# Kernel optimization log

Measured on AMD Instinct MI355X. Metric: run time of the kernel, lower is better.

## Reference

```python
import jax, jax.numpy as jnp
import numpy as np

B, S, V, E, HE, HD, MEL_D, MEL_T = 4096, 13, 276, 128, 256, 256, 80, 250

def setup_inputs() -> dict:
    key = jax.random.key(0)
    ks = jax.random.split(key, 20)
    p = lambda k, sh: (jax.random.normal(k, sh, dtype=jnp.float32) * 0.05)
    return {
        'text': jax.random.randint(ks[0], (B, S), 0, V),
        'surprisal': jax.random.normal(ks[1], (B, S), dtype=jnp.float32),
        'emb': p(ks[2], (V, E)),
        'sw': p(ks[3], (E, 1)), 'sb': p(ks[4], (E,)),
        'ew_ih': p(ks[5], (4 * HE, E)), 'ew_hh': p(ks[6], (4 * HE, HE)),
        'eb_ih': p(ks[7], (4 * HE,)), 'eb_hh': p(ks[8], (4 * HE,)),
        'aw': p(ks[9], (1, HD + HE)), 'ab': p(ks[10], (1,)),
        'dw_ih': p(ks[11], (4 * HD, E + HE)), 'dw_hh': p(ks[12], (4 * HD, HD)),
        'db_ih': p(ks[13], (4 * HD,)), 'db_hh': p(ks[14], (4 * HD,)),
        'f1w': p(ks[15], (1024, S * HD)), 'f1b': p(ks[16], (1024,)),
        'f2w': p(ks[17], (MEL_D * MEL_T, 1024)), 'f2b': p(ks[18], (MEL_D * MEL_T,)),
        'init_in': jnp.zeros((E,), dtype=jnp.float32),
    }

def _lstm_cell(x, h, c, w_ih, w_hh, b_ih, b_hh, H):
    # PyTorch gate order: i, f, g, o
    g = x @ w_ih.T + b_ih + h @ w_hh.T + b_hh
    i, f, gg, o = jnp.split(g, 4, axis=-1)
    c2 = jax.nn.sigmoid(f) * c + jax.nn.sigmoid(i) * jnp.tanh(gg)
    h2 = jax.nn.sigmoid(o) * jnp.tanh(c2)
    return h2, c2

def reference(text, surprisal, emb, sw, sb, ew_ih, ew_hh, eb_ih, eb_hh,
              aw, ab, dw_ih, dw_hh, db_ih, db_hh, f1w, f1b, f2w, f2b, init_in):
    # embedding + surprisal projection
    x = emb[text] + (surprisal[..., None] @ sw.T + sb)  # [B,S,E]

    # encoder LSTM over time
    def enc_step(carry, xt):
        h, c = carry
        h2, c2 = _lstm_cell(xt, h, c, ew_ih, ew_hh, eb_ih, eb_hh, HE)
        return (h2, c2), h2
    h0 = jnp.zeros((B, HE), dtype=x.dtype)
    (h_n, c_n), enc_seq = jax.lax.scan(enc_step, (h0, h0), jnp.swapaxes(x, 0, 1))
    enc_out = jnp.swapaxes(enc_seq, 0, 1)  # [B,S,HE]

    # precompute encoder part of attention scores (constant across steps)
    aw_h, aw_e = aw[0, :HD], aw[0, HD:]
    enc_score = enc_out @ aw_e + ab[0]  # [B,S]

    dec_in = jnp.broadcast_to(init_in, (B, E))

    def dec_step(carry, _):
        h, c = carry
        scores = h @ aw_h + 0.0  # [B]
        w = jax.nn.softmax(scores[:, None] + enc_score, axis=1)  # [B,S]
        context = jnp.einsum('bs,bsh->bh', w, enc_out)
        xcat = jnp.concatenate([dec_in, context], axis=-1)
        h2, c2 = _lstm_cell(xcat, h, c, dw_ih, dw_hh, db_ih, db_hh, HD)
        return (h2, c2), h2
    _, dec_seq = jax.lax.scan(dec_step, (h_n, c_n), None, length=S)
    dec_out = jnp.swapaxes(dec_seq, 0, 1).reshape(B, S * HD)  # [B,13*256]

    hfc = jax.nn.relu(dec_out @ f1w.T + f1b)
    out = (hfc @ f2w.T + f2b).reshape(B, MEL_D, MEL_T)
    return out
```

## Files before the change

kernel.cpp:

```cpp
#include <hip/hip_runtime.h>
#include <hip/hip_bf16.h>
#include <stdint.h>
#include <stddef.h>

#define B 4096
#define S 13
#define NG 1024
#define MEL 20000
#define MELP 20480

typedef __attribute__((ext_vector_type(8))) short bf16x8;
typedef __attribute__((ext_vector_type(4))) float f32x4;

__device__ __forceinline__ void g2l16(void* lds, const void* g) {
    __builtin_amdgcn_global_load_lds(
        (const __attribute__((address_space(1))) void*)g,
        (__attribute__((address_space(3))) void*)lds, 16, 0, 0);
}

__device__ __forceinline__ float sigm(float x) { return 1.0f / (1.0f + expf(-x)); }
__device__ __forceinline__ float b2f(unsigned short u) {
    union { float f; unsigned int i; } x; x.i = ((unsigned)u) << 16; return x.f;
}
__device__ __forceinline__ unsigned short f2bu(float f) {
    __hip_bfloat16 h = __float2bfloat16(f);
    return *reinterpret_cast<unsigned short*>(&h);
}
__device__ __forceinline__ bf16x8 cvt8(f32x4 a, f32x4 b) {
    union { bf16x8 v; __hip_bfloat16 e[8]; } u;
    #pragma unroll
    for (int j = 0; j < 4; ++j) { u.e[j] = __float2bfloat16(a[j]); u.e[4 + j] = __float2bfloat16(b[j]); }
    return u.v;
}

__device__ __forceinline__ void swz_decode(int wg, int nwg, int nx, int& bx, int& by) {
    const int cpx = nwg >> 3;
    wg = (wg & 7) * cpx + (wg >> 3);
    const int gsz = nx * 4;
    const int grp = wg / gsz, rem = wg % gsz;
    by = grp * 4 + (rem & 3);
    bx = rem >> 2;
}

#define BAR() do { asm volatile("" ::: "memory"); \
    __builtin_amdgcn_s_barrier(); \
    __builtin_amdgcn_sched_barrier(0); } while (0)

#define P_DECL() \
    __shared__ __hip_bfloat16 As3[4][128 * 32]; \
    __shared__ __hip_bfloat16 Bs3[4][64 * 32]; \
    const int tid  = threadIdx.x; \
    const int lane = tid & 63; \
    const int wv   = tid >> 6; \
    const int l16  = lane & 15; \
    const int sr   = tid >> 2; \
    const int sc   = (((tid & 3) ^ ((tid >> 3) & 3)) << 3); \
    const int sl   = (((lane >> 4) ^ ((l16 >> 1) & 3)) << 3)

#define STG3(buf, k0) do { \
    g2l16(&As3[buf][sr * 32 + (tid & 3) * 8],         Ag + (size_t)sr * K + (k0) + sc); \
    g2l16(&As3[buf][(sr + 64) * 32 + (tid & 3) * 8],  Ag + (size_t)(sr + 64) * K + (k0) + sc); \
    g2l16(&Bs3[buf][sr * 32 + (tid & 3) * 8],         Wg + (size_t)sr * K + (k0) + sc); } while (0)

#define TILE3(cur, stg, k2, DO_STG) do { \
    const __hip_bfloat16* Ab = As3[cur]; \
    const __hip_bfloat16* Bb = Bs3[cur]; \
    bf16x8 af[2], bfr[4]; \
    _Pragma("unroll") for (int m = 0; m < 2; ++m) \
        af[m] = *(const bf16x8*)(Ab + (wv * 32 + m * 16 + l16) * 32 + sl); \
    _Pragma("unroll") for (int n = 0; n < 4; ++n) \
        bfr[n] = *(const bf16x8*)(Bb + (n * 16 + l16) * 32 + sl); \
    if (DO_STG) STG3(stg, k2); \
    __builtin_amdgcn_s_setprio(1); \
    _Pragma("unroll") for (int m = 0; m < 2; ++m) \
        _Pragma("unroll") for (int n = 0; n < 4; ++n) \
            acc[m][n] = __builtin_amdgcn_mfma_f32_16x16x32_bf16(af[m], bfr[n], acc[m][n], 0, 0, 0); \
    __builtin_amdgcn_s_setprio(0); \
} while (0)

#define PIPELINE(K) do { \
    const int nk = (K) >> 5; \
    STG3(0, 0); \
    STG3(1, 32); \
    STG3(2, 64); \
    asm volatile("s_waitcnt vmcnt(6)" ::: "memory"); \
    BAR(); \
    int cur = 0; \
    for (int t = 0; t < nk - 3; ++t) { \
        const int stg = (cur + 3) & 3; \
        TILE3(cur, stg, (t + 3) << 5, true); \
        asm volatile("s_waitcnt vmcnt(6)" ::: "memory"); \
        BAR(); \
        cur = (cur + 1) & 3; \
    } \
    TILE3(cur, 0, 0, false); \
    asm volatile("s_waitcnt vmcnt(3)" ::: "memory"); \
    BAR(); \
    cur = (cur + 1) & 3; \
    TILE3(cur, 0, 0, false); \
    asm volatile("s_waitcnt vmcnt(0)" ::: "memory"); \
    BAR(); \
    cur = (cur + 1) & 3; \
    TILE3(cur, 0, 0, false); \
} while (0)

__global__ __launch_bounds__(256, 2) void gemm3(
    const __hip_bfloat16* __restrict__ A,
    const __hip_bfloat16* __restrict__ W,
    const float* __restrict__ bias,
    float* __restrict__ Cf,
    __hip_bfloat16* __restrict__ Cbf,
    int N, int K, int ldc, int relu, int nx)
{
    P_DECL();
    int bx, by;
    swz_decode(blockIdx.x, gridDim.x, nx, bx, by);
    const int brow = by * 128, bcol = bx * 64;
    const __hip_bfloat16* Ag = A + (size_t)brow * K;
    const __hip_bfloat16* Wg = W + (size_t)bcol * K;
    f32x4 acc[2][4] = {};

    PIPELINE(K);

    const int r4 = (lane >> 4) * 4;
    #pragma unroll
    for (int m = 0; m < 2; ++m) {
        #pragma unroll
        for (int n = 0; n < 4; ++n) {
            const int col = bcol + n * 16 + l16;
            if (col >= N) continue;
            const float bv = bias ? bias[col] : 0.0f;
            #pragma unroll
            for (int r = 0; r < 4; ++r) {
                const int row = brow + wv * 32 + m * 16 + r4 + r;
                float v = acc[m][n][r] + bv;
                if (relu) v = v > 0.0f ? v : 0.0f;
                if (Cf)  Cf[(size_t)row * ldc + col] = v;
                if (Cbf) Cbf[(size_t)row * ldc + col] = __float2bfloat16(v);
            }
        }
    }
}

__global__ __launch_bounds__(256, 2) void gemm_lstm3(
    const __hip_bfloat16* __restrict__ A,
    const __hip_bfloat16* __restrict__ W,
    const float* __restrict__ bias,
    float* __restrict__ c,
    __hip_bfloat16* __restrict__ hb1, int s1,
    __hip_bfloat16* __restrict__ hb2, int s2,
    int K,
    const float* __restrict__ aw,
    float* __restrict__ score)
{
    P_DECL();
    int bx, by;
    swz_decode(blockIdx.x, gridDim.x, 16, bx, by);
    const int brow = by * 128, bcol = bx * 64;
    const __hip_bfloat16* Ag = A + (size_t)brow * K;
    const __hip_bfloat16* Wg = W + (size_t)bcol * K;
    f32x4 acc[2][4] = {};

    PIPELINE(K);

    const int r4 = (lane >> 4) * 4;
    const int unit = bx * 16 + l16;
    const float b0 = bias[bcol + l16];
    const float b1 = bias[bcol + 16 + l16];
    const float b2 = bias[bcol + 32 + l16];
    const float b3 = bias[bcol + 48 + l16];
    const float awe = score ? aw[256 + unit] : 0.0f;
    float ps[2][4];
    #pragma unroll
    for (int m = 0; m < 2; ++m) {
        #pragma unroll
        for (int r = 0; r < 4; ++r) {
            const int row = brow + wv * 32 + m * 16 + r4 + r;
            const float gi = acc[m][0][r] + b0;
            const float gf = acc[m][1][r] + b1;
            const float gg = acc[m][2][r] + b2;
            const float go = acc[m][3][r] + b3;
            const size_t ci = (size_t)row * 256 + unit;
            const float c2 = sigm(gf) * c[ci] + sigm(gi) * tanhf(gg);
            const float h2 = sigm(go) * tanhf(c2);
            c[ci] = c2;
            ps[m][r] = h2 * awe;
            const __hip_bfloat16 hb = __float2bfloat16(h2);
            hb1[(size_t)row * s1 + unit] = hb;
            hb2[(size_t)row * s2 + unit] = hb;
        }
    }
    if (score) {
        #pragma unroll
        for (int m = 0; m < 2; ++m) {
            #pragma unroll
            for (int r = 0; r < 4; ++r) {
                float v = ps[m][r];
                v += __shfl_xor(v, 1);
                v += __shfl_xor(v, 2);
                v += __shfl_xor(v, 4);
                v += __shfl_xor(v, 8);
                if (l16 == 0) {
                    const int row = brow + wv * 32 + m * 16 + r4 + r;
                    atomicAdd(&score[(size_t)row * S], v);
                }
            }
        }
    }
}

__global__ __launch_bounds__(256, 2) void gemm_lstm_dec(
    const __hip_bfloat16* __restrict__ A,
    const __hip_bfloat16* __restrict__ W,
    const float* __restrict__ gctx,
    float* __restrict__ c,
    __hip_bfloat16* __restrict__ hb1,
    __hip_bfloat16* __restrict__ hb2, int s2,
    int K)
{
    P_DECL();
    int bx, by;
    swz_decode(blockIdx.x, gridDim.x, 16, bx, by);
    const int brow = by * 128, bcol = bx * 64;
    const __hip_bfloat16* Ag = A + (size_t)brow * K;
    const __hip_bfloat16* Wg = W + (size_t)bcol * K;
    f32x4 acc[2][4] = {};

    PIPELINE(K);

    const int r4 = (lane >> 4) * 4;
    const int unit = bx * 16 + l16;
    #pragma unroll
    for (int m = 0; m < 2; ++m) {
        #pragma unroll
        for (int r = 0; r < 4; ++r) {
            const int row = brow + wv * 32 + m * 16 + r4 + r;
            const float* g = gctx + (size_t)row * NG + bcol;
            const float gi = acc[m][0][r] + g[l16];
            const float gf = acc[m][1][r] + g[16 + l16];
            const float gg = acc[m][2][r] + g[32 + l16];
            const float go = acc[m][3][r] + g[48 + l16];
            const size_t ci = (size_t)row * 256 + unit;
            const float c2 = sigm(gf) * c[ci] + sigm(gi) * tanhf(gg);
            const float h2 = sigm(go) * tanhf(c2);
            c[ci] = c2;
            const __hip_bfloat16 hb = __float2bfloat16(h2);
            hb1[(size_t)row * 256 + unit] = hb;
            hb2[(size_t)row * s2 + unit] = hb;
        }
    }
}

__global__ __launch_bounds__(512, 2) void gemm256(
    const __hip_bfloat16* __restrict__ A,
    const __hip_bfloat16* __restrict__ W,
    const float* __restrict__ bias,
    float* __restrict__ Cf,
    int N, int K, int ldc, int nx)
{
    __shared__ __hip_bfloat16 As[4][256 * 32];
    __shared__ __hip_bfloat16 Bs[4][256 * 32];
    const int tid  = threadIdx.x;
    const int lane = tid & 63;
    const int wv = tid >> 6, wr = wv >> 2, wc = wv & 3;
    const int l16 = lane & 15;
    int bx, by;
    {
        const int xcd = blockIdx.x & 7;
        const int lid = blockIdx.x >> 3;
        const int st  = lid >> 4;
        const int w   = lid & 15;
        const int gst = xcd * 10 + st;
        const int sbx = gst >> 2;
        const int sby = gst & 3;
        bx = sbx * 4 + (w & 3);
        by = sby * 4 + (w >> 2);
    }
    const int brow = by * 256, bcol = bx * 256;
    const __hip_bfloat16* Ag = A + (size_t)brow * K;
    const __hip_bfloat16* Wg = W + (size_t)bcol * K;
    const int sr = tid >> 2;
    const int sc = (((tid & 3) ^ ((tid >> 3) & 3)) << 3);
    const int sd = tid * 8;
    const int sl = (((lane >> 4) ^ ((l16 >> 1) & 3)) << 3);
    f32x4 acc[8][4] = {};
    const int nk = K >> 5;

    #define STG_A(buf, k0) do { \
        g2l16(&As[buf][sd],        Ag + (size_t)sr * K + (k0) + sc);         \
        g2l16(&As[buf][4096 + sd], Ag + (size_t)(sr + 128) * K + (k0) + sc); } while (0)
    #define STG_B(buf, k0) do { \
        g2l16(&Bs[buf][sd],        Wg + (size_t)sr * K + (k0) + sc);         \
        g2l16(&Bs[buf][4096 + sd], Wg + (size_t)(sr + 128) * K + (k0) + sc); } while (0)

    #define TILE(cur, stg, k2, DO_STG) do {                                    \
        const __hip_bfloat16* Ab = As[cur];                                    \
        const __hip_bfloat16* Bb = Bs[cur];                                    \
        bf16x8 bfr[4], af[4];                                                  \
        _Pragma("unroll") for (int n = 0; n < 4; ++n)                          \
            bfr[n] = *(const bf16x8*)(Bb + (wc * 64 + n * 16 + l16) * 32 + sl);\
        _Pragma("unroll") for (int m = 0; m < 4; ++m)                          \
            af[m] = *(const bf16x8*)(Ab + (wr * 128 + m * 16 + l16) * 32 + sl);\
        if (DO_STG) STG_A(stg, k2);                                            \
        __builtin_amdgcn_s_setprio(1);                                         \
        _Pragma("unroll") for (int m = 0; m < 4; ++m)                          \
            _Pragma("unroll") for (int n = 0; n < 4; ++n)                      \
                acc[m][n] = __builtin_amdgcn_mfma_f32_16x16x32_bf16(           \
                    af[m], bfr[n], acc[m][n], 0, 0, 0);                        \
        __builtin_amdgcn_s_setprio(0);                                         \
        _Pragma("unroll") for (int m = 0; m < 4; ++m)                          \
            af[m] = *(const bf16x8*)(Ab + (wr * 128 + (m + 4) * 16 + l16) * 32 + sl); \
        if (DO_STG) STG_B(stg, k2);                                            \
        __builtin_amdgcn_s_setprio(1);                                         \
        _Pragma("unroll") for (int m = 0; m < 4; ++m)                          \
            _Pragma("unroll") for (int n = 0; n < 4; ++n)                      \
                acc[m + 4][n] = __builtin_amdgcn_mfma_f32_16x16x32_bf16(       \
                    af[m], bfr[n], acc[m + 4][n], 0, 0, 0);                    \
        __builtin_amdgcn_s_setprio(0);                                         \
    } while (0)

    STG_A(0, 0);  STG_B(0, 0);
    STG_A(1, 32); STG_B(1, 32);
    STG_A(2, 64); STG_B(2, 64);
    asm volatile("s_waitcnt vmcnt(8)" ::: "memory");
    BAR();
    int cur = 0;
    for (int t = 0; t < nk - 3; ++t) {
        const int stg = (cur + 3) & 3;
        TILE(cur, stg, (t + 3) << 5, true);
        asm volatile("s_waitcnt vmcnt(8)" ::: "memory");
        BAR();
        cur = (cur + 1) & 3;
    }
    TILE(cur, 0, 0, false);
    asm volatile("s_waitcnt vmcnt(4)" ::: "memory");
    BAR();
    cur = (cur + 1) & 3;
    TILE(cur, 0, 0, false);
    asm volatile("s_waitcnt vmcnt(0)" ::: "memory");
    BAR();
    cur = (cur + 1) & 3;
    TILE(cur, 0, 0, false);

    const int r4 = (lane >> 4) * 4;
    #pragma unroll
    for (int m = 0; m < 8; ++m) {
        #pragma unroll
        for (int n = 0; n < 4; ++n) {
            const int col = bcol + wc * 64 + n * 16 + l16;
            if (col >= N) continue;
            const float bv = bias[col];
            #pragma unroll
            for (int r = 0; r < 4; ++r) {
                const int row = brow + wr * 128 + m * 16 + r4 + r;
                Cf[(size_t)row * ldc + col] = acc[m][n][r] + bv;
            }
        }
    }
}

__device__ __forceinline__ int unperm(int np) {
    const int u = ((np >> 6) << 4) + (np & 15);
    const int g = (np >> 4) & 3;
    return g * 256 + u;
}

#define N_W2   ((long long)MELP * 1024 / 8)
#define N_W1   ((long long)NG * 3328 / 8)
#define N_WE   ((long long)NG * 384 / 8)
#define N_WD   ((long long)NG * 512 / 8)
#define N_EMB  ((long long)B * S * 32)
#define N_INIT ((long long)B * 256)
#define N_F2B  ((long long)MELP)
#define N_BP   ((long long)NG)
#define N_ES   ((long long)B * S)
#define N_PREP (N_W2 + N_W1 + N_WE + N_WD + N_EMB + N_INIT + N_F2B + N_BP + N_ES)

__global__ void prep_all(
    const int* __restrict__ text, const float* __restrict__ surp,
    const float* __restrict__ emb, const float* __restrict__ sw,
    const float* __restrict__ sb,
    const float* __restrict__ ew_ih, const float* __restrict__ ew_hh,
    const float* __restrict__ eb_ih, const float* __restrict__ eb_hh,
    const float* __restrict__ dw_ih, const float* __restrict__ dw_hh,
    const float* __restrict__ db_ih, const float* __restrict__ db_hh,
    const float* __restrict__ f1w, const float* __restrict__ f2w,
    const float* __restrict__ f2b, const float* __restrict__ init_in,
    const float* __restrict__ ab,
    __hip_bfloat16* __restrict__ Wenc,
    __hip_bfloat16* __restrict__ Wdc, __hip_bfloat16* __restrict__ Wdh,
    __hip_bfloat16* __restrict__ W1, __hip_bfloat16* __restrict__ W2,
    float* __restrict__ f2bp, float* __restrict__ be, float* __restrict__ bd,
    __hip_bfloat16* __restrict__ xall, float* __restrict__ c_buf,
    float* __restrict__ enc_score)
{
    long long id = (long long)blockIdx.x * 256 + threadIdx.x;
    if (id < N_W2) {
        const long long i8 = id * 8;
        bf16x8 v;
        if (i8 < (long long)MEL * 1024) {
            v = cvt8(*(const f32x4*)(f2w + i8), *(const f32x4*)(f2w + i8 + 4));
        } else {
            union { bf16x8 w; __hip_bfloat16 e[8]; } u;
            #pragma unroll
            for (int j = 0; j < 8; ++j) u.e[j] = __float2bfloat16(0.0f);
            v = u.w;
        }
        *(bf16x8*)(W2 + i8) = v;
        return;
    }
    id -= N_W2;
    if (id < N_W1) {
        const long long i8 = id * 8;
        *(bf16x8*)(W1 + i8) = cvt8(*(const f32x4*)(f1w + i8), *(const f32x4*)(f1w + i8 + 4));
        return;
    }
    id -= N_W1;
    if (id < N_WE) {
        const int idx = (int)(id * 8);
        const int np = idx / 384, k = idx % 384;
        const int n = unperm(np);
        const float* src = (k < 128) ? (ew_ih + n * 128 + k) : (ew_hh + n * 256 + (k - 128));
        *(bf16x8*)(Wenc + idx) = cvt8(*(const f32x4*)src, *(const f32x4*)(src + 4));
        return;
    }
    id -= N_WE;
    if (id < N_WD) {
        const int idx = (int)(id * 8);
        const int np = idx / 512, k = idx % 512;
        const int n = unperm(np);
        if (k < 256) {
            const float* src = dw_ih + n * 384 + 128 + k;
            *(bf16x8*)(Wdc + np * 256 + k) = cvt8(*(const f32x4*)src, *(const f32x4*)(src + 4));
        } else {
            const float* src = dw_hh + n * 256 + (k - 256);
            *(bf16x8*)(Wdh + np * 256 + (k - 256)) = cvt8(*(const f32x4*)src, *(const f32x4*)(src + 4));
        }
        return;
    }
    id -= N_WD;
    if (id < N_EMB) {
        const int idx = (int)id;
        const int jj = (idx & 31) * 4;
        const int rest = idx >> 5;
        const int b = rest % B;
        const int s = rest / B;
        const float sp = surp[b * S + s];
        const f32x4 e4 = *(const f32x4*)(emb + (size_t)text[b * S + s] * 128 + jj);
        const f32x4 w4 = *(const f32x4*)(sw + jj);
        const f32x4 b4 = *(const f32x4*)(sb + jj);
        __hip_bfloat16* dst = xall + ((size_t)s * B + b) * 384 + jj;
        #pragma unroll
        for (int i = 0; i < 4; ++i) dst[i] = __float2bfloat16(e4[i] + sp * w4[i] + b4[i]);
        return;
    }
    id -= N_EMB;
    if (id < N_INIT) {
        const int idx = (int)id;
        c_buf[idx] = 0.0f;
        const int b = idx >> 8, jj = idx & 255;
        xall[(size_t)b * 384 + 128 + jj] = __float2bfloat16(0.0f);
        return;
    }
    id -= N_INIT;
    if (id < N_F2B) {
        const int idx = (int)id;
        f2bp[idx] = (idx < MEL) ? f2b[idx] : 0.0f;
        return;
    }
    id -= N_F2B;
    if (id < N_BP) {
        const int np = (int)id;
        const int n = unperm(np);
        be[np] = eb_ih[n] + eb_hh[n];
        float s = db_ih[n] + db_hh[n];
        for (int k = 0; k < 128; ++k) s += dw_ih[n * 384 + k] * init_in[k];
        bd[np] = s;
        return;
    }
    id -= N_BP;
    if (id < N_ES) {
        enc_score[id] = ab[0];
        return;
    }
}

__global__ void attn_once(const __hip_bfloat16* __restrict__ enc_out,
                          const float* __restrict__ enc_score,
                          __hip_bfloat16* __restrict__ ctx) {
    int b = (blockIdx.x * 256 + threadIdx.x) >> 6;
    int lane = threadIdx.x & 63;
    if (b >= B) return;
    float sc[S], mx = -1e30f;
    #pragma unroll
    for (int t = 0; t < S; ++t) { sc[t] = enc_score[b * S + t]; mx = fmaxf(mx, sc[t]); }
    float sum = 0.0f;
    #pragma unroll
    for (int t = 0; t < S; ++t) { sc[t] = expf(sc[t] - mx); sum += sc[t]; }
    const float inv = 1.0f / sum;
    float c0 = 0.f, c1 = 0.f, c2 = 0.f, c3 = 0.f;
    #pragma unroll
    for (int t = 0; t < S; ++t) {
        const ushort4 e4 = *(const ushort4*)(enc_out + ((size_t)b * S + t) * 256 + lane * 4);
        const float w = sc[t] * inv;
        c0 += w * b2f(e4.x); c1 += w * b2f(e4.y);
        c2 += w * b2f(e4.z); c3 += w * b2f(e4.w);
    }
    ushort4 o4 = { f2bu(c0), f2bu(c1), f2bu(c2), f2bu(c3) };
    *(ushort4*)(ctx + (size_t)b * 256 + lane * 4) = o4;
}

#define CDIV(a, b) (((a) + (b) - 1) / (b))

extern "C" void kernel_launch(void* const* d_in, const int* in_sizes, int n_in,
                              void* d_out, int out_size, void* d_ws, size_t ws_size,
                              hipStream_t stream) {
    const int*   text    = (const int*)  d_in[0];
    const float* surp    = (const float*)d_in[1];
    const float* emb     = (const float*)d_in[2];
    const float* sw      = (const float*)d_in[3];
    const float* sb      = (const float*)d_in[4];
    const float* ew_ih   = (const float*)d_in[5];
    const float* ew_hh   = (const float*)d_in[6];
    const float* eb_ih   = (const float*)d_in[7];
    const float* eb_hh   = (const float*)d_in[8];
    const float* aw      = (const float*)d_in[9];
    const float* ab      = (const float*)d_in[10];
    const float* dw_ih   = (const float*)d_in[11];
    const float* dw_hh   = (const float*)d_in[12];
    const float* db_ih   = (const float*)d_in[13];
    const float* db_hh   = (const float*)d_in[14];
    const float* f1w     = (const float*)d_in[15];
    const float* f1b     = (const float*)d_in[16];
    const float* f2w     = (const float*)d_in[17];
    const float* f2b     = (const float*)d_in[18];
    const float* init_in = (const float*)d_in[19];
    float* out = (float*)d_out;

    char* p = (char*)d_ws;
    auto alloc = [&](size_t bytes) {
        void* r = (void*)p;
        p += (bytes + 255) & ~(size_t)255;
        return r;
    };
    __hip_bfloat16* Wenc      = (__hip_bfloat16*)alloc((size_t)NG * 384 * 2);
    __hip_bfloat16* Wdc       = (__hip_bfloat16*)alloc((size_t)NG * 256 * 2);
    __hip_bfloat16* Wdh       = (__hip_bfloat16*)alloc((size_t)NG * 256 * 2);
    __hip_bfloat16* W1        = (__hip_bfloat16*)alloc((size_t)NG * 3328 * 2);
    __hip_bfloat16* W2        = (__hip_bfloat16*)alloc((size_t)MELP * 1024 * 2);
    float*          f2bp      = (float*)alloc((size_t)MELP * 4);
    float*          be        = (float*)alloc((size_t)NG * 4);
    float*          bd        = (float*)alloc((size_t)NG * 4);
    __hip_bfloat16* xall      = (__hip_bfloat16*)alloc((size_t)S * B * 384 * 2);
    __hip_bfloat16* enc_out   = (__hip_bfloat16*)alloc((size_t)B * S * 256 * 2);
    float*          enc_score = (float*)alloc((size_t)B * S * 4);
    float*          c_buf     = (float*)alloc((size_t)B * 256 * 4);
    __hip_bfloat16* ctx       = (__hip_bfloat16*)alloc((size_t)B * 256 * 2);
    float*          gctx      = (float*)alloc((size_t)B * NG * 4);
    __hip_bfloat16* hdec      = (__hip_bfloat16*)alloc((size_t)2 * B * 256 * 2);
    __hip_bfloat16* dec_out   = (__hip_bfloat16*)alloc((size_t)B * 3328 * 2);
    __hip_bfloat16* hfc       = (__hip_bfloat16*)alloc((size_t)B * 1024 * 2);
    (void)ws_size; (void)in_sizes; (void)n_in; (void)out_size;

    prep_all<<<(int)CDIV(N_PREP, 256), 256, 0, stream>>>(
        text, surp, emb, sw, sb, ew_ih, ew_hh, eb_ih, eb_hh,
        dw_ih, dw_hh, db_ih, db_hh, f1w, f2w, f2b, init_in, ab,
        Wenc, Wdc, Wdh, W1, W2, f2bp, be, bd, xall, c_buf, enc_score);

    for (int t = 0; t < S; ++t) {
        __hip_bfloat16* hb1; int s1;
        if (t < S - 1) { hb1 = xall + ((size_t)(t + 1) * B * 384) + 128; s1 = 384; }
        else           { hb1 = hdec; s1 = 256; }
        gemm_lstm3<<<512, 256, 0, stream>>>(
            xall + (size_t)t * B * 384, Wenc, be, c_buf,
            hb1, s1, enc_out + (size_t)t * 256, S * 256, 384,
            aw, enc_score + t);
    }

    attn_once<<<CDIV(B * 64, 256), 256, 0, stream>>>(enc_out, enc_score, ctx);
    gemm3<<<(NG / 64) * (B / 128), 256, 0, stream>>>(
        ctx, Wdc, bd, gctx, (__hip_bfloat16*)nullptr, NG, 256, NG, 0, NG / 64);

    for (int t = 0; t < S; ++t) {
        gemm_lstm_dec<<<512, 256, 0, stream>>>(
            hdec + (size_t)(t & 1) * B * 256, Wdh, gctx, c_buf,
            hdec + (size_t)((t + 1) & 1) * B * 256,
            dec_out + (size_t)t * 256, 3328, 256);
    }

    gemm3<<<(NG / 64) * (B / 128), 256, 0, stream>>>(
        dec_out, W1, f1b, (float*)nullptr, hfc, NG, 3328, NG, 1, NG / 64);

    gemm256<<<(MELP / 256) * (B / 256), 512, 0, stream>>>(
        hfc, W2, f2bp, out, MEL, 1024, MEL, MELP / 256);
}
```

Measured before the change: 596.9 us.

## Restructure GEMM K-loop to process tile pairs with one barrier per pair

Both GEMM main loops now prefetch four K-stages up front, then walk the K dimension two tiles at a time. Each pair restages two buffers, and a single full vmcnt(0) wait plus barrier follows the pair. The aim is to halve the number of barriers and drop the peeled epilogue tiles. The cost is that the prefetch is fully drained every two tiles, so only about one tile of compute hides each load, versus roughly three before. The loop also assumes an even number of K-tiles.

```diff
diff --git a/kernel.cpp b/kernel.cpp
--- a/kernel.cpp
+++ b/kernel.cpp
@@ -83,25 +83,18 @@
     STG3(0, 0); \
     STG3(1, 32); \
     STG3(2, 64); \
+    STG3(3, 96); \
     asm volatile("s_waitcnt vmcnt(6)" ::: "memory"); \
     BAR(); \
-    int cur = 0; \
-    for (int t = 0; t < nk - 3; ++t) { \
-        const int stg = (cur + 3) & 3; \
-        TILE3(cur, stg, (t + 3) << 5, true); \
-        asm volatile("s_waitcnt vmcnt(6)" ::: "memory"); \
+    const int np = nk >> 1; \
+    for (int pp = 0; pp < np; ++pp) { \
+        const int t0 = pp << 1; \
+        const int dos = (pp >= 1) && (t0 + 2 < nk); \
+        TILE3((t0 & 3), ((t0 + 2) & 3), (t0 + 2) << 5, dos); \
+        TILE3(((t0 + 1) & 3), ((t0 + 3) & 3), (t0 + 3) << 5, dos); \
+        asm volatile("s_waitcnt vmcnt(0)" ::: "memory"); \
         BAR(); \
-        cur = (cur + 1) & 3; \
     } \
-    TILE3(cur, 0, 0, false); \
-    asm volatile("s_waitcnt vmcnt(3)" ::: "memory"); \
-    BAR(); \
-    cur = (cur + 1) & 3; \
-    TILE3(cur, 0, 0, false); \
-    asm volatile("s_waitcnt vmcnt(0)" ::: "memory"); \
-    BAR(); \
-    cur = (cur + 1) & 3; \
-    TILE3(cur, 0, 0, false); \
 } while (0)
 
 __global__ __launch_bounds__(256, 2) void gemm3(
@@ -322,25 +315,18 @@
     STG_A(0, 0);  STG_B(0, 0);
     STG_A(1, 32); STG_B(1, 32);
     STG_A(2, 64); STG_B(2, 64);
+    STG_A(3, 96); STG_B(3, 96);
     asm volatile("s_waitcnt vmcnt(8)" ::: "memory");
     BAR();
-    int cur = 0;
-    for (int t = 0; t < nk - 3; ++t) {
-        const int stg = (cur + 3) & 3;
-        TILE(cur, stg, (t + 3) << 5, true);
-        asm volatile("s_waitcnt vmcnt(8)" ::: "memory");
+    const int np = nk >> 1;
+    for (int pp = 0; pp < np; ++pp) {
+        const int t0 = pp << 1;
+        const int dos = (pp >= 1) && (t0 + 2 < nk);
+        TILE((t0 & 3), ((t0 + 2) & 3), (t0 + 2) << 5, dos);
+        TILE(((t0 + 1) & 3), ((t0 + 3) & 3), (t0 + 3) << 5, dos);
+        asm volatile("s_waitcnt vmcnt(0)" ::: "memory");
         BAR();
-        cur = (cur + 1) & 3;
-    }
-    TILE(cur, 0, 0, false);
-    asm volatile("s_waitcnt vmcnt(4)" ::: "memory");
-    BAR();
-    cur = (cur + 1) & 3;
-    TILE(cur, 0, 0, false);
-    asm volatile("s_waitcnt vmcnt(0)" ::: "memory");
-    BAR();
-    cur = (cur + 1) & 3;
-    TILE(cur, 0, 0, false);
+    }
 
     const int r4 = (lane >> 4) * 4;
     #pragma unroll
```

Measured after the change: 601.7 us. About the same (+0.8%).
